# Kernel optimization log

Hardware: AMD Instinct MI355X
Metric: run time of the kernel (lower is better)

## Reference

```python
import jax, jax.numpy as jnp
import numpy as np

B, S, C, L, H = 128, 8, 120, 469, 64


def setup_inputs() -> dict:
    key = jax.random.key(0)
    kx, kk, kq, kv = jax.random.split(key, 4)
    scale = 1.0 / np.sqrt(L)
    x = jax.random.normal(kx, (B, S, C, L), dtype=jnp.float32)
    # nn.Linear(L, H, bias=False): y = x @ W^T with W:[H,L]; store as [L,H] so y = x @ W
    Wk = jax.random.normal(kk, (L, H), dtype=jnp.float32) * scale
    Wq = jax.random.normal(kq, (L, H), dtype=jnp.float32) * scale
    Wv = jax.random.normal(kv, (L, H), dtype=jnp.float32) * scale
    return {"x": x, "Wk": Wk, "Wq": Wq, "Wv": Wv}


def reference(x, Wk, Wq, Wv):
    b, s, c, l = x.shape
    h = Wk.shape[-1]
    # torch: x.view(S_, B, C_, L_) -- a raw reshape, not a permute
    xs = x.reshape(s, b, c, l)
    k = xs @ Wk  # (s, b, c, h)
    q = xs @ Wq
    v = xs @ Wv
    wei = jnp.einsum('sbch,sbdh->sbcd', q, k) * (h ** -0.5)
    wei = jax.nn.softmax(wei, axis=-1)  # dropout = identity in eval
    out = jnp.einsum('sbcd,sbdh->sbch', wei, v)  # (s, b, c, h)
    # torch: matrices.view(B, S_, C_, head_size) -- raw reshape again
    return out.reshape(b, s, c, h)
```

## Files before the change

kernel.cpp:

```cpp
#include <hip/hip_runtime.h>

typedef __attribute__((ext_vector_type(8))) short bf16x8;
typedef __attribute__((ext_vector_type(4))) float f32x4;
typedef unsigned short ushort_t;

#define BB 128
#define SS 8
#define CC 120
#define LL 469
#define HH 64

constexpr int NBATCH = SS * BB;
constexpr int KSTEPS = (LL + 31) / 32;

constexpr int XBUF_FLOATS = 128 * 32;
constexpr int XBUF_BYTES  = XBUF_FLOATS * 4;
constexpr int WBUF_SHORTS = 192 * 40;
constexpr int WBUF_BYTES  = WBUF_SHORTS * 2;
constexpr int SMEM_BYTES  = 2 * XBUF_BYTES + 2 * WBUF_BYTES;
constexpr int WIMG_BYTES  = KSTEPS * WBUF_BYTES;

__device__ __forceinline__ ushort_t f2bf(float f) {
  union { float f; unsigned u; } v; v.f = f;
  unsigned r = (v.u + 0x7FFFu + ((v.u >> 16) & 1u)) >> 16;
  return (ushort_t)r;
}

__device__ __forceinline__ void gload_lds4(const void* g, void* l) {
  __builtin_amdgcn_global_load_lds(
      (const __attribute__((address_space(1))) unsigned int*)g,
      (__attribute__((address_space(3))) unsigned int*)l, 4, 0, 0);
}
__device__ __forceinline__ void gload_lds16(const void* g, void* l) {
  __builtin_amdgcn_global_load_lds(
      (const __attribute__((address_space(1))) unsigned int*)g,
      (__attribute__((address_space(3))) unsigned int*)l, 16, 0, 0);
}

__device__ __forceinline__ char* sptr(char* base, int row, int stride, int byteoff) {
  return base + row * stride + (byteoff ^ ((row & 7) << 4));
}

__global__ void prep_w(const float* __restrict__ Wk, const float* __restrict__ Wq,
                       const float* __restrict__ Wv, ushort_t* __restrict__ wimg) {
  int idx = blockIdx.x * 256 + threadIdx.x;
  int t = idx / (192 * 40);
  int rem = idx % (192 * 40);
  int col = rem / 40;
  int kk = rem % 40;
  int k = t * 32 + kk;
  int wsel = col >> 6, h = col & 63;
  const float* wp = (wsel == 0) ? Wk : (wsel == 1) ? Wq : Wv;
  float v = (kk < 32 && k < LL) ? wp[(size_t)k * HH + h] : 0.f;
  wimg[idx] = f2bf(v);
}

template <bool WIMG>
__global__ __launch_bounds__(256, 2)
void fused_regional_head(const float* __restrict__ x,
                         const float* __restrict__ Wk,
                         const float* __restrict__ Wq,
                         const float* __restrict__ Wv,
                         const ushort_t* __restrict__ wimg,
                         float* __restrict__ out) {
  __shared__ char smem[SMEM_BYTES];
  const int tid = threadIdx.x;
  const int lane = tid & 63;
  const int wv = tid >> 6;
  const int lr = lane & 15;
  const int lg = lane >> 4;
  const int batch = blockIdx.x;
  const size_t xbase = (size_t)batch * CC * LL;

  float* Xf = (float*)smem;
  ushort_t* Wl = (ushort_t*)(smem + 2 * XBUF_BYTES);

  Xf[0 * XBUF_FLOATS + 120 * 32 + tid] = 0.f;
  Xf[1 * XBUF_FLOATS + 120 * 32 + tid] = 0.f;

  auto stage_x = [&](int buf, int t) {
    const int k0 = t * 32;
    float* dst = Xf + buf * XBUF_FLOATS;
#pragma unroll
    for (int i = 0; i < 15; ++i) {
      int slot = i * 4 + wv;
      int dw = slot * 64 + lane;
      int row = dw >> 5;
      int w = dw & 31;
      int s = w >> 2, q = w & 3;
      int lw = ((s ^ (row & 7)) << 2) | q;
      int k = k0 + lw;
      if (k < LL) {
        gload_lds4(x + xbase + (size_t)row * LL + k, dst + slot * 64);
      } else {
        dst[dw] = 0.f;
      }
    }
  };

  auto stage_w = [&](int buf, int t) {
    ushort_t* wb = Wl + buf * WBUF_SHORTS;
    if constexpr (WIMG) {
      const char* src = (const char*)(wimg + t * WBUF_SHORTS);
#pragma unroll
      for (int i = 0; i < 4; ++i) {
        int c = wv + 4 * i;
        if (c < 15) gload_lds16(src + c * 1024 + lane * 16, (char*)wb + c * 1024);
      }
    } else {
      const int k0 = t * 32;
#pragma unroll
      for (int j = 0; j < 24; ++j) {
        int idx = j * 256 + tid;
        int col = idx >> 5, kk = idx & 31;
        int k = k0 + kk;
        int wsel = col >> 6, h = col & 63;
        const float* wp = (wsel == 0) ? Wk : (wsel == 1) ? Wq : Wv;
        float v = (k < LL) ? wp[(size_t)k * HH + h] : 0.f;
        wb[col * 40 + kk] = f2bf(v);
      }
    }
  };

  auto loadA = [&](const float* xb, int row) -> bf16x8 {
    int s0 = (lg * 2) ^ (row & 7);
    int s1 = (lg * 2 + 1) ^ (row & 7);
    f32x4 c0 = *(const f32x4*)(xb + row * 32 + s0 * 4);
    f32x4 c1 = *(const f32x4*)(xb + row * 32 + s1 * 4);
    bf16x8 r;
    r[0] = (short)f2bf(c0[0]); r[1] = (short)f2bf(c0[1]);
    r[2] = (short)f2bf(c0[2]); r[3] = (short)f2bf(c0[3]);
    r[4] = (short)f2bf(c1[0]); r[5] = (short)f2bf(c1[1]);
    r[6] = (short)f2bf(c1[2]); r[7] = (short)f2bf(c1[3]);
    return r;
  };

  f32x4 acc[2][12];
#pragma unroll
  for (int m = 0; m < 2; ++m)
#pragma unroll
    for (int n = 0; n < 12; ++n) acc[m][n] = (f32x4){0.f, 0.f, 0.f, 0.f};

  stage_x(0, 0);
  stage_w(0, 0);
  for (int t = 0; t < KSTEPS; ++t) {
    __syncthreads();
    if (t + 1 < KSTEPS) { stage_x((t + 1) & 1, t + 1); stage_w((t + 1) & 1, t + 1); }
    const float* xb = Xf + (t & 1) * XBUF_FLOATS;
    const ushort_t* wb = Wl + (t & 1) * WBUF_SHORTS;
    bf16x8 a0 = loadA(xb, wv * 32 + lr);
    bf16x8 a1 = loadA(xb, wv * 32 + 16 + lr);
#pragma unroll
    for (int n = 0; n < 12; ++n) {
      bf16x8 b = *(const bf16x8*)(wb + (n * 16 + lr) * 40 + lg * 8);
      acc[0][n] = __builtin_amdgcn_mfma_f32_16x16x32_bf16(a0, b, acc[0][n], 0, 0, 0);
      acc[1][n] = __builtin_amdgcn_mfma_f32_16x16x32_bf16(a1, b, acc[1][n], 0, 0, 0);
    }
  }
  __syncthreads();

  char* Qb = smem;
  char* Kb = smem + 16384;
  char* Vb = smem + 32768;
  char* Pb = smem;
#pragma unroll
  for (int mt = 0; mt < 2; ++mt)
#pragma unroll
    for (int r = 0; r < 4; ++r) {
      int row = wv * 32 + mt * 16 + lg * 4 + r;
#pragma unroll
      for (int n = 0; n < 4; ++n) {
        *(ushort_t*)sptr(Kb, row, 128, (n * 16 + lr) * 2) = f2bf(acc[mt][n][r]);
        *(ushort_t*)sptr(Qb, row, 128, (n * 16 + lr) * 2) = f2bf(acc[mt][4 + n][r]);
        *(ushort_t*)sptr(Vb, n * 16 + lr, 256, row * 2) = f2bf(acc[mt][8 + n][r]);
      }
    }
  __syncthreads();

  f32x4 accw[2][8];
#pragma unroll
  for (int m = 0; m < 2; ++m)
#pragma unroll
    for (int n = 0; n < 8; ++n) accw[m][n] = (f32x4){0.f, 0.f, 0.f, 0.f};
#pragma unroll
  for (int ks = 0; ks < 2; ++ks) {
    bf16x8 a0 = *(const bf16x8*)sptr(Qb, wv * 32 + lr, 128, ks * 64 + lg * 16);
    bf16x8 a1 = *(const bf16x8*)sptr(Qb, wv * 32 + 16 + lr, 128, ks * 64 + lg * 16);
#pragma unroll
    for (int n = 0; n < 8; ++n) {
      bf16x8 b = *(const bf16x8*)sptr(Kb, n * 16 + lr, 128, ks * 64 + lg * 16);
      accw[0][n] = __builtin_amdgcn_mfma_f32_16x16x32_bf16(a0, b, accw[0][n], 0, 0, 0);
      accw[1][n] = __builtin_amdgcn_mfma_f32_16x16x32_bf16(a1, b, accw[1][n], 0, 0, 0);
    }
  }
  __syncthreads();

  const float sc = 0.125f;
#pragma unroll
  for (int mt = 0; mt < 2; ++mt)
#pragma unroll
    for (int r = 0; r < 4; ++r) {
      float l[8];
      float m = -1e30f;
#pragma unroll
      for (int n = 0; n < 8; ++n) {
        float v = accw[mt][n][r] * sc;
        if (n == 7 && lr >= 8) v = -1e30f;
        l[n] = v;
        m = fmaxf(m, v);
      }
#pragma unroll
      for (int off = 1; off < 16; off <<= 1) m = fmaxf(m, __shfl_xor(m, off));
      float s = 0.f;
#pragma unroll
      for (int n = 0; n < 8; ++n) {
        float p = __expf(l[n] - m);
        l[n] = p;
        s += p;
      }
#pragma unroll
      for (int off = 1; off < 16; off <<= 1) s += __shfl_xor(s, off);
      float inv = 1.f / s;
      int row = wv * 32 + mt * 16 + lg * 4 + r;
#pragma unroll
      for (int n = 0; n < 8; ++n)
        *(ushort_t*)sptr(Pb, row, 256, (n * 16 + lr) * 2) = f2bf(l[n] * inv);
    }

  f32x4 acco[2][4];
#pragma unroll
  for (int m = 0; m < 2; ++m)
#pragma unroll
    for (int n = 0; n < 4; ++n) acco[m][n] = (f32x4){0.f, 0.f, 0.f, 0.f};
#pragma unroll
  for (int ks = 0; ks < 4; ++ks) {
    bf16x8 a0 = *(const bf16x8*)sptr(Pb, wv * 32 + lr, 256, ks * 64 + lg * 16);
    bf16x8 a1 = *(const bf16x8*)sptr(Pb, wv * 32 + 16 + lr, 256, ks * 64 + lg * 16);
#pragma unroll
    for (int n = 0; n < 4; ++n) {
      bf16x8 b = *(const bf16x8*)sptr(Vb, n * 16 + lr, 256, ks * 64 + lg * 16);
      acco[0][n] = __builtin_amdgcn_mfma_f32_16x16x32_bf16(a0, b, acco[0][n], 0, 0, 0);
      acco[1][n] = __builtin_amdgcn_mfma_f32_16x16x32_bf16(a1, b, acco[1][n], 0, 0, 0);
    }
  }

  const size_t obase = (size_t)batch * CC * HH;
#pragma unroll
  for (int mt = 0; mt < 2; ++mt)
#pragma unroll
    for (int r = 0; r < 4; ++r) {
      int row = wv * 32 + mt * 16 + lg * 4 + r;
      if (row < CC) {
#pragma unroll
        for (int n = 0; n < 4; ++n)
          out[obase + (size_t)row * HH + n * 16 + lr] = acco[mt][n][r];
      }
    }
}

extern "C" void kernel_launch(void* const* d_in, const int* in_sizes, int n_in,
                              void* d_out, int out_size, void* d_ws, size_t ws_size,
                              hipStream_t stream) {
  (void)in_sizes; (void)n_in; (void)out_size;
  const float* x  = (const float*)d_in[0];
  const float* Wk = (const float*)d_in[1];
  const float* Wq = (const float*)d_in[2];
  const float* Wv = (const float*)d_in[3];
  float* out = (float*)d_out;
  if (ws_size >= (size_t)WIMG_BYTES && d_ws != nullptr) {
    ushort_t* wimg = (ushort_t*)d_ws;
    prep_w<<<450, 256, 0, stream>>>(Wk, Wq, Wv, wimg);
    fused_regional_head<true><<<NBATCH, 256, 0, stream>>>(x, Wk, Wq, Wv, wimg, out);
  } else {
    fused_regional_head<false><<<NBATCH, 256, 0, stream>>>(x, Wk, Wq, Wv, nullptr, out);
  }
}
```

Baseline: 77.27 us.

## Single-buffer X tile to cut LDS and raise occupancy; vectorize V and output stores

Reduces the X staging to one buffer sized for the 120 real rows. The fp32 A fragments are read into registers before an extra barrier, and only then is the next X tile staged into the same buffer. This cuts LDS to 48KB so launch bounds can ask for three blocks per CU. V fragments are now packed into 4-wide stores, and the output goes through LDS so it can be written with coalesced float4 global stores. The cost is an extra barrier per K step, less overlap between X loading and compute, and a switch to the library bf16 conversion.

Result: slower. 129.2 us (+67.2%).

```diff
diff --git a/kernel.cpp b/kernel.cpp
--- a/kernel.cpp
+++ b/kernel.cpp
@@ -1,7 +1,9 @@
 #include <hip/hip_runtime.h>
+#include <hip/hip_bf16.h>
 
 typedef __attribute__((ext_vector_type(8))) short bf16x8;
 typedef __attribute__((ext_vector_type(4))) float f32x4;
+typedef __attribute__((ext_vector_type(4))) short short4v;
 typedef unsigned short ushort_t;
 
 #define BB 128
@@ -13,17 +15,16 @@
 constexpr int NBATCH = SS * BB;
 constexpr int KSTEPS = (LL + 31) / 32;
 
-constexpr int XBUF_FLOATS = 128 * 32;
+constexpr int XBUF_FLOATS = 120 * 32;
 constexpr int XBUF_BYTES  = XBUF_FLOATS * 4;
 constexpr int WBUF_SHORTS = 192 * 40;
 constexpr int WBUF_BYTES  = WBUF_SHORTS * 2;
-constexpr int SMEM_BYTES  = 2 * XBUF_BYTES + 2 * WBUF_BYTES;
+constexpr int SMEM_BYTES  = 49152;
 constexpr int WIMG_BYTES  = KSTEPS * WBUF_BYTES;
 
 __device__ __forceinline__ ushort_t f2bf(float f) {
-  union { float f; unsigned u; } v; v.f = f;
-  unsigned r = (v.u + 0x7FFFu + ((v.u >> 16) & 1u)) >> 16;
-  return (ushort_t)r;
+  __hip_bfloat16 h = __float2bfloat16(f);
+  return __builtin_bit_cast(ushort_t, h);
 }
 
 __device__ __forceinline__ void gload_lds4(const void* g, void* l) {
@@ -56,7 +57,7 @@
 }
 
 template <bool WIMG>
-__global__ __launch_bounds__(256, 2)
+__global__ __launch_bounds__(256, 3)
 void fused_regional_head(const float* __restrict__ x,
                          const float* __restrict__ Wk,
                          const float* __restrict__ Wq,
@@ -73,14 +74,10 @@
   const size_t xbase = (size_t)batch * CC * LL;
 
   float* Xf = (float*)smem;
-  ushort_t* Wl = (ushort_t*)(smem + 2 * XBUF_BYTES);
-
-  Xf[0 * XBUF_FLOATS + 120 * 32 + tid] = 0.f;
-  Xf[1 * XBUF_FLOATS + 120 * 32 + tid] = 0.f;
-
-  auto stage_x = [&](int buf, int t) {
+  ushort_t* Wl = (ushort_t*)(smem + XBUF_BYTES);
+
+  auto stage_x = [&](int t) {
     const int k0 = t * 32;
-    float* dst = Xf + buf * XBUF_FLOATS;
 #pragma unroll
     for (int i = 0; i < 15; ++i) {
       int slot = i * 4 + wv;
@@ -90,11 +87,8 @@
       int s = w >> 2, q = w & 3;
       int lw = ((s ^ (row & 7)) << 2) | q;
       int k = k0 + lw;
-      if (k < LL) {
-        gload_lds4(x + xbase + (size_t)row * LL + k, dst + slot * 64);
-      } else {
-        dst[dw] = 0.f;
-      }
+      if (k < LL) gload_lds4(x + xbase + (size_t)row * LL + k, Xf + slot * 64);
+      else Xf[dw] = 0.f;
     }
   };
 
@@ -122,34 +116,34 @@
     }
   };
 
-  auto loadA = [&](const float* xb, int row) -> bf16x8 {
-    int s0 = (lg * 2) ^ (row & 7);
-    int s1 = (lg * 2 + 1) ^ (row & 7);
-    f32x4 c0 = *(const f32x4*)(xb + row * 32 + s0 * 4);
-    f32x4 c1 = *(const f32x4*)(xb + row * 32 + s1 * 4);
-    bf16x8 r;
-    r[0] = (short)f2bf(c0[0]); r[1] = (short)f2bf(c0[1]);
-    r[2] = (short)f2bf(c0[2]); r[3] = (short)f2bf(c0[3]);
-    r[4] = (short)f2bf(c1[0]); r[5] = (short)f2bf(c1[1]);
-    r[6] = (short)f2bf(c1[2]); r[7] = (short)f2bf(c1[3]);
-    return r;
-  };
-
   f32x4 acc[2][12];
 #pragma unroll
   for (int m = 0; m < 2; ++m)
 #pragma unroll
     for (int n = 0; n < 12; ++n) acc[m][n] = (f32x4){0.f, 0.f, 0.f, 0.f};
 
-  stage_x(0, 0);
+  stage_x(0);
   stage_w(0, 0);
+  const int row0 = wv * 32 + lr;
+  const int row1 = wv * 32 + 16 + lr;
+  const bool r1ok = row1 < CC;
   for (int t = 0; t < KSTEPS; ++t) {
     __syncthreads();
-    if (t + 1 < KSTEPS) { stage_x((t + 1) & 1, t + 1); stage_w((t + 1) & 1, t + 1); }
-    const float* xb = Xf + (t & 1) * XBUF_FLOATS;
+    f32x4 z = (f32x4){0.f, 0.f, 0.f, 0.f};
+    f32x4 c00 = *(const f32x4*)(Xf + row0 * 32 + ((lg * 2) ^ (row0 & 7)) * 4);
+    f32x4 c01 = *(const f32x4*)(Xf + row0 * 32 + ((lg * 2 + 1) ^ (row0 & 7)) * 4);
+    f32x4 c10 = r1ok ? *(const f32x4*)(Xf + row1 * 32 + ((lg * 2) ^ (row1 & 7)) * 4) : z;
+    f32x4 c11 = r1ok ? *(const f32x4*)(Xf + row1 * 32 + ((lg * 2 + 1) ^ (row1 & 7)) * 4) : z;
+    if (t + 1 < KSTEPS) stage_w((t + 1) & 1, t + 1);
+    __syncthreads();
+    if (t + 1 < KSTEPS) stage_x(t + 1);
+    bf16x8 a0, a1;
+#pragma unroll
+    for (int j = 0; j < 4; ++j) {
+      a0[j] = (short)f2bf(c00[j]); a0[4 + j] = (short)f2bf(c01[j]);
+      a1[j] = (short)f2bf(c10[j]); a1[4 + j] = (short)f2bf(c11[j]);
+    }
     const ushort_t* wb = Wl + (t & 1) * WBUF_SHORTS;
-    bf16x8 a0 = loadA(xb, wv * 32 + lr);
-    bf16x8 a1 = loadA(xb, wv * 32 + 16 + lr);
 #pragma unroll
     for (int n = 0; n < 12; ++n) {
       bf16x8 b = *(const bf16x8*)(wb + (n * 16 + lr) * 40 + lg * 8);
@@ -164,7 +158,7 @@
   char* Vb = smem + 32768;
   char* Pb = smem;
 #pragma unroll
-  for (int mt = 0; mt < 2; ++mt)
+  for (int mt = 0; mt < 2; ++mt) {
 #pragma unroll
     for (int r = 0; r < 4; ++r) {
       int row = wv * 32 + mt * 16 + lg * 4 + r;
@@ -172,9 +166,16 @@
       for (int n = 0; n < 4; ++n) {
         *(ushort_t*)sptr(Kb, row, 128, (n * 16 + lr) * 2) = f2bf(acc[mt][n][r]);
         *(ushort_t*)sptr(Qb, row, 128, (n * 16 + lr) * 2) = f2bf(acc[mt][4 + n][r]);
-        *(ushort_t*)sptr(Vb, n * 16 + lr, 256, row * 2) = f2bf(acc[mt][8 + n][r]);
-      }
-    }
+      }
+    }
+#pragma unroll
+    for (int n = 0; n < 4; ++n) {
+      short4v pk;
+#pragma unroll
+      for (int r = 0; r < 4; ++r) pk[r] = (short)f2bf(acc[mt][8 + n][r]);
+      *(short4v*)sptr(Vb, n * 16 + lr, 256, (wv * 32 + mt * 16 + lg * 4) * 2) = pk;
+    }
+  }
   __syncthreads();
 
   f32x4 accw[2][8];
@@ -195,7 +196,6 @@
   }
   __syncthreads();
 
-  const float sc = 0.125f;
 #pragma unroll
   for (int mt = 0; mt < 2; ++mt)
 #pragma unroll
@@ -204,7 +204,7 @@
       float m = -1e30f;
 #pragma unroll
       for (int n = 0; n < 8; ++n) {
-        float v = accw[mt][n][r] * sc;
+        float v = accw[mt][n][r] * 0.125f;
         if (n == 7 && lr >= 8) v = -1e30f;
         l[n] = v;
         m = fmaxf(m, v);
@@ -244,7 +244,8 @@
     }
   }
 
-  const size_t obase = (size_t)batch * CC * HH;
+  __syncthreads();
+  float* Ob = (float*)smem;
 #pragma unroll
   for (int mt = 0; mt < 2; ++mt)
 #pragma unroll
@@ -253,9 +254,21 @@
       if (row < CC) {
 #pragma unroll
         for (int n = 0; n < 4; ++n)
-          out[obase + (size_t)row * HH + n * 16 + lr] = acco[mt][n][r];
-      }
-    }
+          Ob[row * 68 + n * 16 + lr] = acco[mt][n][r];
+      }
+    }
+  __syncthreads();
+  const size_t obase = (size_t)batch * CC * HH;
+#pragma unroll
+  for (int i = 0; i < 8; ++i) {
+    int idx = i * 256 + tid;
+    if (idx < 1920) {
+      int row = idx >> 4;
+      int c4 = (idx & 15) * 4;
+      f32x4 v = *(const f32x4*)(Ob + row * 68 + c4);
+      *(f32x4*)(out + obase + (size_t)idx * 4) = v;
+    }
+  }
 }
 
 extern "C" void kernel_launch(void* const* d_in, const int* in_sizes, int n_in,
```
